# Optimization experiments

Measured on AMD Instinct MI355X. Metric: run time of the kernel, lower is better.

Reference implementation:

```python
import jax, jax.numpy as jnp
import numpy as np
from jax import lax

IMG = 256   # model img_size
O = 7       # adaptive pool output size (out_size)
R = 32      # number of ROIs
B = 8       # batch
CF = 32     # UNet output channels
FOUT = 512  # fc out_features


def _conv(x, w, b):
    y = lax.conv_general_dilated(x, w, (1, 1), 'SAME',
                                 dimension_numbers=('NCHW', 'OIHW', 'NCHW'))
    return y + b[None, :, None, None]


def _pool(x):
    return lax.reduce_window(x, -jnp.inf, lax.max, (1, 1, 2, 2), (1, 1, 2, 2), 'VALID')


def _up(x):
    return jnp.repeat(jnp.repeat(x, 2, axis=2), 2, axis=3)


def _unet(x, p):
    r = jax.nn.relu
    e1 = r(_conv(r(_conv(x, p['e1w1'], p['e1b1'])), p['e1w2'], p['e1b2']))          # [B,32,H,W]
    e2 = r(_conv(r(_conv(_pool(e1), p['e2w1'], p['e2b1'])), p['e2w2'], p['e2b2']))  # [B,64,H/2,W/2]
    bo = r(_conv(r(_conv(_pool(e2), p['bw1'], p['bb1'])), p['bw2'], p['bb2']))      # [B,128,H/4,W/4]
    u2 = r(_conv(_up(bo), p['u2w'], p['u2b']))                                      # [B,64,H/2,W/2]
    d2 = r(_conv(r(_conv(jnp.concatenate([u2, e2], 1), p['d2w1'], p['d2b1'])), p['d2w2'], p['d2b2']))
    u1 = r(_conv(_up(d2), p['u1w'], p['u1b']))                                      # [B,32,H,W]
    d1 = r(_conv(r(_conv(jnp.concatenate([u1, e1], 1), p['d1w1'], p['d1b1'])), p['d1w2'], p['d1b2']))
    return _conv(d1, p['fw'], p['fb'])                                              # [B,CF,H,W]


def _adaptive_pool(ii, boxes):
    # Exact F.adaptive_avg_pool2d bins via an integral image.
    # ii: [B,C,H+1,W+1] (zero-padded 2D cumsum); boxes: [R,4] int (x1,y1,x2,y2).
    i = jnp.arange(O)
    h = boxes[:, 3] - boxes[:, 1]
    w = boxes[:, 2] - boxes[:, 0]
    sy = boxes[:, 1:2] + (i[None, :] * h[:, None]) // O            # floor(i*h/O)
    ey = boxes[:, 1:2] + ((i[None, :] + 1) * h[:, None] + O - 1) // O  # ceil((i+1)*h/O)
    sx = boxes[:, 0:1] + (i[None, :] * w[:, None]) // O
    ex = boxes[:, 0:1] + ((i[None, :] + 1) * w[:, None] + O - 1) // O
    yA, yB = sy[:, :, None], ey[:, :, None]   # [R,O,1]
    xA, xB = sx[:, None, :], ex[:, None, :]   # [R,1,O]
    s = ii[:, :, yB, xB] - ii[:, :, yA, xB] - ii[:, :, yB, xA] + ii[:, :, yA, xA]  # [B,C,R,O,O]
    area = ((ey - sy)[:, :, None] * (ex - sx)[:, None, :]).astype(ii.dtype)        # [R,O,O]
    return s / area[None, None]


def _forward(x, rois, p):
    H, W = x.shape[2], x.shape[3]
    xs, ys = IMG // H, IMG // W  # matches torch: x_scale, y_scale = img_size//m, img_size//n
    boxes = rois // jnp.array([xs, ys, xs, ys], dtype=rois.dtype)
    f = _unet(x, p)                                   # [B,CF,H,W]
    ii = jnp.pad(jnp.cumsum(jnp.cumsum(f, axis=2), axis=3),
                 ((0, 0), (0, 0), (1, 0), (1, 0)))    # integral image [B,CF,H+1,W+1]
    rp = _adaptive_pool(ii, boxes)                    # [B,CF,R,O,O]
    roi_feat = jnp.transpose(rp, (0, 2, 1, 3, 4)).reshape(x.shape[0], boxes.shape[0] * f.shape[1], O, O)
    gbox = jnp.array([[0, 0, W, H]], dtype=boxes.dtype)
    gpool = _adaptive_pool(ii, gbox)[:, :, 0]         # [B,CF,O,O]
    out = jnp.concatenate([gpool, roi_feat], axis=1)  # [B,(R+1)*CF,O,O]
    out = out.reshape(out.shape[0], out.shape[1], O * O)
    return jnp.einsum('bnk,fk->bnf', out, p['fcw']) + p['fcb']


_PNAMES = ['e1w1','e1b1','e1w2','e1b2','e2w1','e2b1','e2w2','e2b2','bw1','bb1','bw2','bb2',
           'u2w','u2b','d2w1','d2b1','d2w2','d2b2','u1w','u1b','d1w1','d1b1','d1w2','d1b2',
           'fw','fb','fcw','fcb']


def setup_inputs() -> dict:
    key = jax.random.key(0)
    ks = jax.random.split(key, 32)

    def w(k, shape):
        fan = int(np.prod(shape[1:]))
        return jax.random.normal(k, shape, jnp.float32) * np.sqrt(2.0 / fan)

    d = {}
    d['x'] = jax.random.normal(ks[0], (B, 3, IMG, IMG), jnp.float32)
    xy1 = jax.random.randint(ks[1], (R, 2), 0, 192)
    wh = jax.random.randint(ks[2], (R, 2), 16, 64)
    d['rois'] = jnp.concatenate([xy1, xy1 + wh], axis=1).astype(jnp.int32)  # (x1,y1,x2,y2)

    shapes = {'e1w1': (32, 3, 3, 3), 'e1w2': (32, 32, 3, 3),
              'e2w1': (64, 32, 3, 3), 'e2w2': (64, 64, 3, 3),
              'bw1': (128, 64, 3, 3), 'bw2': (128, 128, 3, 3),
              'u2w': (64, 128, 3, 3),
              'd2w1': (64, 128, 3, 3), 'd2w2': (64, 64, 3, 3),
              'u1w': (32, 64, 3, 3),
              'd1w1': (32, 64, 3, 3), 'd1w2': (32, 32, 3, 3),
              'fw': (CF, 32, 1, 1),
              'fcw': (FOUT, O * O)}
    i = 3
    for n, s in shapes.items():
        d[n] = w(ks[i], s); i += 1
        bn = n.replace('w', 'b', 1) if 'w' in n else n
        d[bn] = jnp.zeros((s[0],), jnp.float32)
    d['fcb'] = jnp.zeros((FOUT,), jnp.float32)
    return d


def reference(x, rois, e1w1, e1b1, e1w2, e1b2, e2w1, e2b1, e2w2, e2b2,
              bw1, bb1, bw2, bb2, u2w, u2b, d2w1, d2b1, d2w2, d2b2,
              u1w, u1b, d1w1, d1b1, d1w2, d1b2, fw, fb, fcw, fcb):
    p = dict(e1w1=e1w1, e1b1=e1b1, e1w2=e1w2, e1b2=e1b2, e2w1=e2w1, e2b1=e2b1,
             e2w2=e2w2, e2b2=e2b2, bw1=bw1, bb1=bb1, bw2=bw2, bb2=bb2,
             u2w=u2w, u2b=u2b, d2w1=d2w1, d2b1=d2b1, d2w2=d2w2, d2b2=d2b2,
             u1w=u1w, u1b=u1b, d1w1=d1w1, d1b1=d1b1, d1w2=d1w2, d1b2=d1b2,
             fw=fw, fb=fb, fcw=fcw, fcb=fcb)
    return _forward(x, rois, p)
```

## Files before the change

kernel.cpp:

```cpp
#include <hip/hip_runtime.h>

typedef _Float16 half8 __attribute__((ext_vector_type(8)));
typedef float f32x4 __attribute__((ext_vector_type(4)));
typedef float f32x16 __attribute__((ext_vector_type(16)));

__device__ __forceinline__ unsigned short f2h(float f) {
    _Float16 h = (_Float16)f;
    return __builtin_bit_cast(unsigned short, h);
}
__device__ __forceinline__ float h2f(unsigned short u) {
    return (float)__builtin_bit_cast(_Float16, u);
}

__device__ __forceinline__ void lds_load16(const uint4* g, uint4* l) {
    __builtin_amdgcn_global_load_lds(
        (const __attribute__((address_space(1))) unsigned int*)g,
        (__attribute__((address_space(3))) unsigned int*)l, 16, 0, 0);
}

struct PrepArgs {
    const float* src[13];
    unsigned dstOff[13];
    int Cout[13], Cin[13];
    unsigned off[14];
};

__global__ void prep_all_k(PrepArgs a, char* __restrict__ WT)
{
    unsigned t = blockIdx.x * 256 + threadIdx.x;
    if (t >= a.off[13]) return;
    int l = 0;
    while (t >= a.off[l + 1]) ++l;
    unsigned e = t - a.off[l];
    if (l < 11) {
        int j = e & 7; unsigned r = e >> 3;
        const int Cout = a.Cout[l], Cin = a.Cin[l];
        int co = r % Cout; r /= Cout;
        int oct = r & 3; r >>= 2;
        int pos = r % 9; int ck = r / 9;
        int ci = ck * 32 + oct * 8 + j;
        ((unsigned short*)(WT + a.dstOff[l]))[e] =
            f2h(a.src[l][((size_t)co * Cin + ci) * 9 + pos]);
    } else if (l == 11) {
        int k = e >> 9, ff = e & 511;
        ((float*)(WT + a.dstOff[l]))[e] = a.src[l][ff * 49 + k];
    } else {
        int j = e & 7, co = (e >> 3) & 31, koct = e >> 8;
        ((unsigned short*)(WT + a.dstOff[l]))[e] =
            f2h(a.src[l][co * 32 + koct * 8 + j]);
    }
}

template<int BM, int TW, int TH, int LW, int UP, int POOL>
__global__ __launch_bounds__(256, 2) void convm4_k(
    const uint4* __restrict__ in1, int C1g,
    const uint4* __restrict__ in2, int C2g,
    const uint4* __restrict__ wt,
    const float* __restrict__ bias,
    unsigned short* __restrict__ out,
    int Cout, int relu, const uint4* __restrict__ zp,
    unsigned short* __restrict__ pout)
{
    constexpr int NM = BM / 16;
    constexpr int NN = (TW * TH) / 64;
    constexpr int CG = TW / 16;
    constexpr int RQ = NN / CG;
    static_assert(RQ == 2, "row-reuse layout needs 2 rows/wave");
    constexpr int Wf = 1 << LW, Hf = Wf;
    constexpr int WC = TW + 2, HR = TH + 2;
    constexpr int IN_GR = 4 * HR * WC;
    constexpr int LTW = (TW == 64) ? 6 : 5;
    constexpr int sH = UP ? (Hf >> 1) : Hf;
    constexpr int sW = UP ? (Wf >> 1) : Wf;
    __shared__ uint4 smem[IN_GR + 36 * BM];

    const int tid = threadIdx.x;
    const int lane = tid & 63, wv = tid >> 6;
    const int ng = Cout / BM;
    const int b = blockIdx.z / ng, cg = blockIdx.z % ng;
    const int x0 = blockIdx.x * TW, y0 = blockIdx.y * TH;
    const int NCK = (C1g + C2g) / 4;

    f32x4 acc[NM][NN];
#pragma unroll
    for (int m = 0; m < NM; ++m)
#pragma unroll
        for (int n = 0; n < NN; ++n) acc[m][n] = (f32x4){0.f, 0.f, 0.f, 0.f};

    const int l15 = lane & 15, l4 = lane >> 4;
    const int laneB = l4 * HR * WC + l15;
    const int laneA = l4 * BM + l15;

    for (int ck = 0; ck < NCK; ++ck) {
        if (ck) __syncthreads();
        {
            const uint4* src; int cg0, srcCg;
            if (ck * 4 < C1g) { src = in1; cg0 = ck * 4; srcCg = C1g; }
            else              { src = in2; cg0 = ck * 4 - C1g; srcCg = C2g; }
            for (int i = tid; i < IN_GR; i += 256) {
                int oct = i / (HR * WC);
                int rem = i - oct * (HR * WC);
                int row = rem / WC;
                int col = rem - row * WC;
                int gy = y0 + row - 1, gx = x0 + col - 1;
                int sy = UP ? (gy >> 1) : gy, sx = UP ? (gx >> 1) : gx;
                const uint4* ga = ((unsigned)gy < (unsigned)Hf && (unsigned)gx < (unsigned)Wf)
                    ? src + ((((size_t)b * sH + sy) * sW + sx) * srcCg + cg0 + oct)
                    : zp + (i & 63);
                lds_load16(ga, &smem[i]);
            }
        }
        {
            const uint4* wck = wt + (size_t)ck * 36 * Cout + (size_t)cg * BM;
            for (int i = tid; i < 36 * BM; i += 256) {
                int seg = i / BM, col = i - seg * BM;
                lds_load16(wck + seg * Cout + col, &smem[IN_GR + i]);
            }
        }
        __syncthreads();
        const half8* sB = (const half8*)smem;
        const half8* sA = (const half8*)(smem + IN_GR);
#pragma unroll
        for (int dc = 0; dc < 3; ++dc) {
            half8 br[RQ + 2][CG];
#pragma unroll
            for (int r = 0; r < RQ + 2; ++r)
#pragma unroll
                for (int c2 = 0; c2 < CG; ++c2)
                    br[r][c2] = sB[(wv * RQ + r) * WC + c2 * 16 + dc + laneB];
#pragma unroll
            for (int dr = 0; dr < 3; ++dr) {
                half8 af[NM];
#pragma unroll
                for (int m = 0; m < NM; ++m)
                    af[m] = sA[(dr * 3 + dc) * 4 * BM + m * 16 + laneA];
#pragma unroll
                for (int m = 0; m < NM; ++m)
#pragma unroll
                    for (int rq = 0; rq < RQ; ++rq)
#pragma unroll
                        for (int c2 = 0; c2 < CG; ++c2)
                            acc[m][rq * CG + c2] = __builtin_amdgcn_mfma_f32_16x16x32_f16(
                                af[m], br[rq + dr][c2], acc[m][rq * CG + c2], 0, 0, 0);
            }
        }
    }

#pragma unroll
    for (int m = 0; m < NM; ++m) {
        const int co0 = cg * BM + m * 16 + l4 * 4;
        const float4 bs = *(const float4*)(bias + co0);
#pragma unroll
        for (int c2 = 0; c2 < CG; ++c2) {
            float pv0, pv1, pv2, pv3;
#pragma unroll
            for (int rq = 0; rq < RQ; ++rq) {
                const int n = rq * CG + c2;
                const int pix = wv * (NN * 16) + n * 16 + l15;
                const int y = y0 + (pix >> LTW), x = x0 + (pix & (TW - 1));
                float v0 = acc[m][n][0] + bs.x;
                float v1 = acc[m][n][1] + bs.y;
                float v2 = acc[m][n][2] + bs.z;
                float v3 = acc[m][n][3] + bs.w;
                if (relu) {
                    v0 = fmaxf(v0, 0.f); v1 = fmaxf(v1, 0.f);
                    v2 = fmaxf(v2, 0.f); v3 = fmaxf(v3, 0.f);
                }
                uint2 pk;
                pk.x = (unsigned)f2h(v0) | ((unsigned)f2h(v1) << 16);
                pk.y = (unsigned)f2h(v2) | ((unsigned)f2h(v3) << 16);
                *(uint2*)(out + (((size_t)b * Hf + y) * Wf + x) * Cout + co0) = pk;
                if (POOL) {
                    if (rq == 0) { pv0 = v0; pv1 = v1; pv2 = v2; pv3 = v3; }
                    else {
                        pv0 = fmaxf(pv0, v0); pv1 = fmaxf(pv1, v1);
                        pv2 = fmaxf(pv2, v2); pv3 = fmaxf(pv3, v3);
                    }
                }
            }
            if (POOL) {
                float q0 = fmaxf(pv0, __shfl_xor(pv0, 1));
                float q1 = fmaxf(pv1, __shfl_xor(pv1, 1));
                float q2 = fmaxf(pv2, __shfl_xor(pv2, 1));
                float q3 = fmaxf(pv3, __shfl_xor(pv3, 1));
                if ((l15 & 1) == 0) {
                    const int xp = (x0 >> 1) + ((c2 * 16 + l15) >> 1);
                    const int yp = (y0 >> 1) + wv;
                    uint2 pk;
                    pk.x = (unsigned)f2h(q0) | ((unsigned)f2h(q1) << 16);
                    pk.y = (unsigned)f2h(q2) | ((unsigned)f2h(q3) << 16);
                    *(uint2*)(pout + (((size_t)b * (Hf >> 1) + yp) * (Wf >> 1) + xp) * Cout + co0) = pk;
                }
            }
        }
    }
}

__global__ __launch_bounds__(256) void conv0_k(
    const float* __restrict__ in, const float* __restrict__ w,
    const float* __restrict__ bias, unsigned short* __restrict__ out)
{
    __shared__ float s_in[3][18][18];
    const int tx = threadIdx.x, ty = threadIdx.y;
    const int tid = ty * 16 + tx;
    const int b = blockIdx.z >> 2;
    const int coBase = (blockIdx.z & 3) * 8;
    const int bx = blockIdx.x * 16, by = blockIdx.y * 16;

    for (int i = tid; i < 3 * 18 * 18; i += 256) {
        int cc = i / 324, r = i % 324;
        int ly = r / 18, lx = r % 18;
        int gy = by + ly - 1, gx = bx + lx - 1;
        float v = 0.f;
        if ((unsigned)gy < 256u && (unsigned)gx < 256u)
            v = in[(((size_t)(b * 3 + cc)) << 16) + (gy << 8) + gx];
        ((float*)s_in)[i] = v;
    }
    __syncthreads();
    float acc[8];
#pragma unroll
    for (int k = 0; k < 8; ++k) acc[k] = 0.f;
    for (int cc = 0; cc < 3; ++cc) {
        float v[9];
#pragma unroll
        for (int dh = 0; dh < 3; ++dh)
#pragma unroll
            for (int dw = 0; dw < 3; ++dw)
                v[dh * 3 + dw] = s_in[cc][ty + dh][tx + dw];
        const float* wp = w + ((size_t)coBase * 3 + cc) * 9;
#pragma unroll
        for (int k = 0; k < 8; ++k) {
            const float* wk = wp + (size_t)k * 27;
            float a = acc[k];
#pragma unroll
            for (int j = 0; j < 9; ++j) a = fmaf(v[j], wk[j], a);
            acc[k] = a;
        }
    }
    const int h = by + ty, ww = bx + tx;
    unsigned short* op = out + (((size_t)(b * 256 + h)) * 256 + ww) * 32 + coBase;
#pragma unroll
    for (int k = 0; k < 8; ++k)
        op[k] = f2h(fmaxf(acc[k] + bias[coBase + k], 0.f));
}

__global__ __launch_bounds__(256) void conv1x1f_k(
    const uint4* __restrict__ in, const uint4* __restrict__ w16,
    const float* __restrict__ bias, unsigned short* __restrict__ f)
{
    __shared__ uint4 sIn[1024];
    __shared__ uint4 sW[128];
    __shared__ float sb[32];
    const int tid = threadIdx.x;
    const int lane = tid & 63, wv = tid >> 6;
    const int l31 = lane & 31, l5 = lane >> 5;
    const int y = blockIdx.x, b = blockIdx.y;

    const uint4* ip = in + (((size_t)b * 256 + y) * 256) * 4;
#pragma unroll
    for (int it = 0; it < 4; ++it)
        lds_load16(ip + tid + it * 256, &sIn[tid + it * 256]);
    if (tid < 128) lds_load16(w16 + tid, &sW[tid]);
    if (tid < 32) sb[tid] = bias[tid];
    __syncthreads();

    const half8* hW = (const half8*)sW;
    const half8* hIn = (const half8*)sIn;
    half8 af0 = hW[l5 * 32 + l31];
    half8 af1 = hW[(2 + l5) * 32 + l31];
    unsigned short* fp_ = f + ((size_t)b * 32) * 65536 + (size_t)y * 256;
#pragma unroll
    for (int g = 0; g < 2; ++g) {
        const int p0 = wv * 64 + g * 32;
        half8 bf0 = hIn[(p0 + l31) * 4 + l5];
        half8 bf1 = hIn[(p0 + l31) * 4 + 2 + l5];
        f32x16 acc;
#pragma unroll
        for (int q = 0; q < 16; ++q) acc[q] = 0.f;
        acc = __builtin_amdgcn_mfma_f32_32x32x16_f16(af0, bf0, acc, 0, 0, 0);
        acc = __builtin_amdgcn_mfma_f32_32x32x16_f16(af1, bf1, acc, 0, 0, 0);
#pragma unroll
        for (int r = 0; r < 16; ++r) {
            const int co = (r & 3) + 8 * (r >> 2) + 4 * l5;
            fp_[(size_t)co * 65536 + p0 + l31] = f2h(acc[r] + sb[co]);
        }
    }
}

__global__ __launch_bounds__(256) void gcol_k(
    const unsigned short* __restrict__ f, float* __restrict__ colsumG)
{
    const int ki = blockIdx.x;
    const int c  = blockIdx.y;
    const int b  = blockIdx.z;
    const int x  = threadIdx.x;
    const int sy = (ki * 256) / 7, ey = ((ki + 1) * 256 + 6) / 7;
    const unsigned short* pl = f + (size_t)(b * 32 + c) * 65536;
    float s = 0.f;
    for (int y = sy; y < ey; ++y)
        s += h2f(pl[(size_t)y * 256 + x]);
    colsumG[((size_t)(b * 32 + c) * 7 + ki) * 256 + x] = s;
}

__global__ __launch_bounds__(64) void gpool2_k(
    const float* __restrict__ colsumG, float* __restrict__ pooled)
{
    const int c = blockIdx.x, b = blockIdx.y;
    const int lane = threadIdx.x;
    if (lane >= 49) return;
    const int ki = lane / 7, kj = lane % 7;
    const int sy = (ki * 256) / 7, ey = ((ki + 1) * 256 + 6) / 7;
    const int sx = (kj * 256) / 7, ex = ((kj + 1) * 256 + 6) / 7;
    const float* cs = colsumG + ((size_t)(b * 32 + c) * 7 + ki) * 256;
    float s = 0.f;
    for (int x = sx; x < ex; ++x) s += cs[x];
    pooled[((size_t)b * 1056 + c) * 49 + lane] = s / (float)((ey - sy) * (ex - sx));
}

__global__ __launch_bounds__(64) void roi_k(
    const unsigned short* __restrict__ f, const int* __restrict__ rois,
    float* __restrict__ pooled)
{
    __shared__ float colsum[7][64];
    const int n = 32 + blockIdx.x, b = blockIdx.y;
    const int lane = threadIdx.x;
    const int r = (n - 32) >> 5;
    const int c = (n - 32) & 31;
    const int x1 = rois[r * 4 + 0], y1 = rois[r * 4 + 1];
    const int x2 = rois[r * 4 + 2], y2 = rois[r * 4 + 3];
    const int h = y2 - y1, w = x2 - x1;
    const unsigned short* pl = f + (size_t)(b * 32 + c) * 65536;
    if (lane < w) {
        const int x = x1 + lane;
#pragma unroll
        for (int ki = 0; ki < 7; ++ki) {
            const int sy = y1 + (ki * h) / 7, ey = y1 + ((ki + 1) * h + 6) / 7;
            float s = 0.f;
            for (int y = sy; y < ey; ++y)
                s += h2f(pl[(size_t)y * 256 + x]);
            colsum[ki][lane] = s;
        }
    }
    __syncthreads();
    if (lane >= 49) return;
    const int ki = lane / 7, kj = lane % 7;
    const int sy = y1 + (ki * h) / 7, ey = y1 + ((ki + 1) * h + 6) / 7;
    const int sxo = (kj * w) / 7, exo = ((kj + 1) * w + 6) / 7;
    float s = 0.f;
    for (int j = sxo; j < exo; ++j) s += colsum[ki][j];
    pooled[((size_t)b * 1056 + n) * 49 + lane] = s / (float)((ey - sy) * (exo - sxo));
}

__global__ __launch_bounds__(512) void fc_k(
    const float* __restrict__ pooled, const float* __restrict__ fcwT,
    const float* __restrict__ fcb, float* __restrict__ out)
{
    const int nt = blockIdx.x, b = blockIdx.y;
    const int f = threadIdx.x;
    float wr[49];
#pragma unroll
    for (int k = 0; k < 49; ++k) wr[k] = fcwT[k * 512 + f];
    const float base = fcb[f];
    const float* pr = pooled + ((size_t)b * 1056 + nt * 16) * 49;
    float* op = out + (((size_t)b * 1056 + nt * 16)) * 512 + f;
#pragma unroll
    for (int j = 0; j < 16; ++j) {
        float a = base;
#pragma unroll
        for (int k = 0; k < 49; ++k)
            a = fmaf(pr[j * 49 + k], wr[k], a);
        op[(size_t)j * 512] = a;
    }
}

extern "C" void kernel_launch(void* const* d_in, const int* in_sizes, int n_in,
                              void* d_out, int out_size, void* d_ws, size_t ws_size,
                              hipStream_t stream)
{
    const float* x    = (const float*)d_in[0];
    const int*   rois = (const int*)d_in[1];
    const float* e1w1 = (const float*)d_in[2];
    const float* e1b1 = (const float*)d_in[3];
    const float* e1w2 = (const float*)d_in[4];
    const float* e1b2 = (const float*)d_in[5];
    const float* e2w1 = (const float*)d_in[6];
    const float* e2b1 = (const float*)d_in[7];
    const float* e2w2 = (const float*)d_in[8];
    const float* e2b2 = (const float*)d_in[9];
    const float* bw1  = (const float*)d_in[10];
    const float* bb1  = (const float*)d_in[11];
    const float* bw2  = (const float*)d_in[12];
    const float* bb2  = (const float*)d_in[13];
    const float* u2w  = (const float*)d_in[14];
    const float* u2b  = (const float*)d_in[15];
    const float* d2w1 = (const float*)d_in[16];
    const float* d2b1 = (const float*)d_in[17];
    const float* d2w2 = (const float*)d_in[18];
    const float* d2b2 = (const float*)d_in[19];
    const float* u1w  = (const float*)d_in[20];
    const float* u1b  = (const float*)d_in[21];
    const float* d1w1 = (const float*)d_in[22];
    const float* d1b1 = (const float*)d_in[23];
    const float* d1w2 = (const float*)d_in[24];
    const float* d1b2 = (const float*)d_in[25];
    const float* fw   = (const float*)d_in[26];
    const float* fb   = (const float*)d_in[27];
    const float* fcw  = (const float*)d_in[28];
    const float* fcb  = (const float*)d_in[29];

    char* wsb = (char*)d_ws;
    char* WT = wsb;
    char* A  = wsb + 4194304;
    char* D  = A + 33554432;
    char* E  = D + 16777216;
    char* Bb = E + 16777216;
    char* C  = Bb + 33554432;
    char* F  = C + 8388608;
    float* fcwT   = (float*)(WT + 1179648);
    unsigned short* fw16 = (unsigned short*)(WT + 2097152);
    uint4* zp     = (uint4*)(WT + 4194304 - 8192);
    unsigned short* fpl = (unsigned short*)F;
    float* pooled = (float*)C;
    float* colsumG = (float*)(C + 2097152);
    hipMemsetAsync(zp, 0, 8192, stream);

    const float* wsrc[11] = {e1w2, e2w1, e2w2, bw1, bw2, u2w, d2w1, d2w2, u1w, d1w1, d1w2};
    const int wco[11] = {32, 64, 64, 128, 128, 64, 64, 64, 32, 32, 32};
    const int wci[11] = {32, 32, 64, 64, 128, 128, 128, 64, 64, 64, 32};
    size_t woff[11]; size_t o = 0;
    PrepArgs pa;
    unsigned eoff = 0;
    for (int i = 0; i < 11; ++i) {
        woff[i] = o; o += (size_t)wco[i] * wci[i] * 18;
        pa.src[i] = wsrc[i]; pa.dstOff[i] = (unsigned)woff[i];
        pa.Cout[i] = wco[i]; pa.Cin[i] = wci[i];
        pa.off[i] = eoff; eoff += (unsigned)(wco[i] * wci[i] * 9);
    }
    pa.src[11] = fcw; pa.dstOff[11] = 1179648; pa.Cout[11] = 0; pa.Cin[11] = 0;
    pa.off[11] = eoff; eoff += 49 * 512;
    pa.src[12] = fw; pa.dstOff[12] = 2097152; pa.Cout[12] = 0; pa.Cin[12] = 0;
    pa.off[12] = eoff; eoff += 4096;
    pa.off[13] = eoff;
    hipLaunchKernelGGL(prep_all_k, dim3((eoff + 255) / 256), dim3(256), 0, stream, pa, WT);
    auto WP = [&](int i) { return (const uint4*)(WT + woff[i]); };

    #define CV1(i1,C1,i2,C2,wi,bs,ot,Cout,up,rl,pl,po) \
        hipLaunchKernelGGL((convm4_k<32,32,8,8,up,pl>), dim3(8,32,8*((Cout)/32)), dim3(256), 0, stream, \
            (const uint4*)(i1), (C1)/8, (const uint4*)(i2), (C2)/8, WP(wi), bs, \
            (unsigned short*)(ot), Cout, rl, zp, (unsigned short*)(po))
    #define CV2(i1,C1,i2,C2,wi,bs,ot,Cout,up,rl,pl,po) \
        hipLaunchKernelGGL((convm4_k<64,32,8,7,up,pl>), dim3(4,16,8*((Cout)/64)), dim3(256), 0, stream, \
            (const uint4*)(i1), (C1)/8, (const uint4*)(i2), (C2)/8, WP(wi), bs, \
            (unsigned short*)(ot), Cout, rl, zp, (unsigned short*)(po))
    #define CV3(i1,C1,i2,C2,wi,bs,ot,Cout,up,rl) \
        hipLaunchKernelGGL((convm4_k<32,32,8,6,up,0>), dim3(2,8,8*((Cout)/32)), dim3(256), 0, stream, \
            (const uint4*)(i1), (C1)/8, (const uint4*)(i2), (C2)/8, WP(wi), bs, \
            (unsigned short*)(ot), Cout, rl, zp, (unsigned short*)nullptr)

    hipLaunchKernelGGL(conv0_k, dim3(16, 16, 32), dim3(16, 16), 0, stream,
                       x, e1w1, e1b1, (unsigned short*)A);
    CV1(A, 32, nullptr, 0, 0, e1b2, Bb, 32, 0, 1, 1, C);
    CV2(C, 32, nullptr, 0, 1, e2b1, A, 64, 0, 1, 0, nullptr);
    CV2(A, 64, nullptr, 0, 2, e2b2, D, 64, 0, 1, 1, C);
    CV3(C, 64, nullptr, 0, 3, bb1, E, 128, 0, 1);
    CV3(E, 128, nullptr, 0, 4, bb2, A, 128, 0, 1);
    CV2(A, 128, nullptr, 0, 5, u2b, E, 64, 1, 1, 0, nullptr);
    CV2(E, 64, D, 64, 6, d2b1, A, 64, 0, 1, 0, nullptr);
    CV2(A, 64, nullptr, 0, 7, d2b2, D, 64, 0, 1, 0, nullptr);
    CV1(D, 64, nullptr, 0, 8, u1b, A, 32, 1, 1, 0, nullptr);
    CV1(A, 32, Bb, 32, 9, d1b1, D, 32, 0, 1, 0, nullptr);
    CV1(D, 32, nullptr, 0, 10, d1b2, Bb, 32, 0, 1, 0, nullptr);
    hipLaunchKernelGGL(conv1x1f_k, dim3(256, 8), dim3(256), 0, stream,
                       (const uint4*)Bb, (const uint4*)fw16, fb, fpl);
    hipLaunchKernelGGL(gcol_k, dim3(7, 32, 8), dim3(256), 0, stream, fpl, colsumG);
    hipLaunchKernelGGL(roi_k, dim3(1024, 8), dim3(64), 0, stream, fpl, rois, pooled);
    hipLaunchKernelGGL(gpool2_k, dim3(32, 8), dim3(64), 0, stream, colsumG, pooled);
    hipLaunchKernelGGL(fc_k, dim3(66, 8), dim3(512), 0, stream,
                       pooled, fcwT, fcb, (float*)d_out);
    #undef CV1
    #undef CV2
    #undef CV3
}
```

Baseline: 354.0 us.

## Double-buffer LDS staging in conv kernel and shrink BM for mid layers

Adds a DB template flag to the MFMA conv kernel so the next channel chunk's input tile and weights are issued into a second LDS buffer while the current chunk is computed. The aim is to hide global-to-LDS load latency behind MFMA work. Layers with several channel chunks now use the double-buffered variant, and the 64-channel mid layers switch from BM=64 to BM=32 to keep LDS usage down and launch more blocks. The cost is double the LDS footprint, which may lower occupancy. The async loads into the other buffer also rely on the end-of-iteration barrier to be complete before that buffer is read.

```diff
diff --git a/kernel.cpp b/kernel.cpp
--- a/kernel.cpp
+++ b/kernel.cpp
@@ -51,8 +51,8 @@
     }
 }
 
-template<int BM, int TW, int TH, int LW, int UP, int POOL>
-__global__ __launch_bounds__(256, 2) void convm4_k(
+template<int BM, int TW, int TH, int LW, int UP, int POOL, int DB>
+__global__ __launch_bounds__(256, 2) void convm5_k(
     const uint4* __restrict__ in1, int C1g,
     const uint4* __restrict__ in2, int C2g,
     const uint4* __restrict__ wt,
@@ -69,10 +69,13 @@
     constexpr int Wf = 1 << LW, Hf = Wf;
     constexpr int WC = TW + 2, HR = TH + 2;
     constexpr int IN_GR = 4 * HR * WC;
+    constexpr int WT_GR = 36 * BM;
+    constexpr int CHUNK = IN_GR + WT_GR;
     constexpr int LTW = (TW == 64) ? 6 : 5;
     constexpr int sH = UP ? (Hf >> 1) : Hf;
     constexpr int sW = UP ? (Wf >> 1) : Wf;
-    __shared__ uint4 smem[IN_GR + 36 * BM];
+    constexpr int NBUF = DB ? 2 : 1;
+    __shared__ uint4 smem[NBUF][CHUNK];
 
     const int tid = threadIdx.x;
     const int lane = tid & 63, wv = tid >> 6;
@@ -91,35 +94,36 @@
     const int laneB = l4 * HR * WC + l15;
     const int laneA = l4 * BM + l15;
 
+    auto stage = [&](int ck, int par) {
+        const uint4* src; int cg0, srcCg;
+        if (ck * 4 < C1g) { src = in1; cg0 = ck * 4; srcCg = C1g; }
+        else              { src = in2; cg0 = ck * 4 - C1g; srcCg = C2g; }
+        for (int i = tid; i < IN_GR; i += 256) {
+            int oct = i / (HR * WC);
+            int rem = i - oct * (HR * WC);
+            int row = rem / WC;
+            int col = rem - row * WC;
+            int gy = y0 + row - 1, gx = x0 + col - 1;
+            int sy = UP ? (gy >> 1) : gy, sx = UP ? (gx >> 1) : gx;
+            const uint4* ga = ((unsigned)gy < (unsigned)Hf && (unsigned)gx < (unsigned)Wf)
+                ? src + ((((size_t)b * sH + sy) * sW + sx) * srcCg + cg0 + oct)
+                : zp + (i & 63);
+            lds_load16(ga, &smem[par][i]);
+        }
+        const uint4* wck = wt + (size_t)ck * 36 * Cout + (size_t)cg * BM;
+        for (int i = tid; i < WT_GR; i += 256) {
+            int seg = i / BM, col = i - seg * BM;
+            lds_load16(wck + seg * Cout + col, &smem[par][IN_GR + i]);
+        }
+    };
+
+    stage(0, 0);
+    __syncthreads();
     for (int ck = 0; ck < NCK; ++ck) {
-        if (ck) __syncthreads();
-        {
-            const uint4* src; int cg0, srcCg;
-            if (ck * 4 < C1g) { src = in1; cg0 = ck * 4; srcCg = C1g; }
-            else              { src = in2; cg0 = ck * 4 - C1g; srcCg = C2g; }
-            for (int i = tid; i < IN_GR; i += 256) {
-                int oct = i / (HR * WC);
-                int rem = i - oct * (HR * WC);
-                int row = rem / WC;
-                int col = rem - row * WC;
-                int gy = y0 + row - 1, gx = x0 + col - 1;
-                int sy = UP ? (gy >> 1) : gy, sx = UP ? (gx >> 1) : gx;
-                const uint4* ga = ((unsigned)gy < (unsigned)Hf && (unsigned)gx < (unsigned)Wf)
-                    ? src + ((((size_t)b * sH + sy) * sW + sx) * srcCg + cg0 + oct)
-                    : zp + (i & 63);
-                lds_load16(ga, &smem[i]);
-            }
-        }
-        {
-            const uint4* wck = wt + (size_t)ck * 36 * Cout + (size_t)cg * BM;
-            for (int i = tid; i < 36 * BM; i += 256) {
-                int seg = i / BM, col = i - seg * BM;
-                lds_load16(wck + seg * Cout + col, &smem[IN_GR + i]);
-            }
-        }
-        __syncthreads();
-        const half8* sB = (const half8*)smem;
-        const half8* sA = (const half8*)(smem + IN_GR);
+        const int par = DB ? (ck & 1) : 0;
+        if (DB && ck + 1 < NCK) stage(ck + 1, par ^ 1);
+        const half8* sB = (const half8*)smem[par];
+        const half8* sA = (const half8*)(smem[par] + IN_GR);
 #pragma unroll
         for (int dc = 0; dc < 3; ++dc) {
             half8 br[RQ + 2][CG];
@@ -143,6 +147,10 @@
                             acc[m][rq * CG + c2] = __builtin_amdgcn_mfma_f32_16x16x32_f16(
                                 af[m], br[rq + dr][c2], acc[m][rq * CG + c2], 0, 0, 0);
             }
+        }
+        if (ck + 1 < NCK) {
+            if (!DB) { __syncthreads(); stage(ck + 1, 0); }
+            __syncthreads();
         }
     }
 
@@ -444,32 +452,40 @@
     hipLaunchKernelGGL(prep_all_k, dim3((eoff + 255) / 256), dim3(256), 0, stream, pa, WT);
     auto WP = [&](int i) { return (const uint4*)(WT + woff[i]); };
 
-    #define CV1(i1,C1,i2,C2,wi,bs,ot,Cout,up,rl,pl,po) \
-        hipLaunchKernelGGL((convm4_k<32,32,8,8,up,pl>), dim3(8,32,8*((Cout)/32)), dim3(256), 0, stream, \
+    #define CV1S(i1,C1,i2,C2,wi,bs,ot,Cout,up,rl,pl,po) \
+        hipLaunchKernelGGL((convm5_k<32,32,8,8,up,pl,0>), dim3(8,32,8*((Cout)/32)), dim3(256), 0, stream, \
             (const uint4*)(i1), (C1)/8, (const uint4*)(i2), (C2)/8, WP(wi), bs, \
             (unsigned short*)(ot), Cout, rl, zp, (unsigned short*)(po))
-    #define CV2(i1,C1,i2,C2,wi,bs,ot,Cout,up,rl,pl,po) \
-        hipLaunchKernelGGL((convm4_k<64,32,8,7,up,pl>), dim3(4,16,8*((Cout)/64)), dim3(256), 0, stream, \
+    #define CV1D(i1,C1,i2,C2,wi,bs,ot,Cout,up,rl,pl,po) \
+        hipLaunchKernelGGL((convm5_k<32,32,8,8,up,pl,1>), dim3(8,32,8*((Cout)/32)), dim3(256), 0, stream, \
             (const uint4*)(i1), (C1)/8, (const uint4*)(i2), (C2)/8, WP(wi), bs, \
             (unsigned short*)(ot), Cout, rl, zp, (unsigned short*)(po))
-    #define CV3(i1,C1,i2,C2,wi,bs,ot,Cout,up,rl) \
-        hipLaunchKernelGGL((convm4_k<32,32,8,6,up,0>), dim3(2,8,8*((Cout)/32)), dim3(256), 0, stream, \
+    #define CV2S(i1,C1,i2,C2,wi,bs,ot,Cout,up,rl,pl,po) \
+        hipLaunchKernelGGL((convm5_k<64,32,8,7,up,pl,0>), dim3(4,16,8*((Cout)/64)), dim3(256), 0, stream, \
+            (const uint4*)(i1), (C1)/8, (const uint4*)(i2), (C2)/8, WP(wi), bs, \
+            (unsigned short*)(ot), Cout, rl, zp, (unsigned short*)(po))
+    #define CV2D(i1,C1,i2,C2,wi,bs,ot,Cout,up,rl,pl,po) \
+        hipLaunchKernelGGL((convm5_k<32,32,8,7,up,pl,1>), dim3(4,16,8*((Cout)/32)), dim3(256), 0, stream, \
+            (const uint4*)(i1), (C1)/8, (const uint4*)(i2), (C2)/8, WP(wi), bs, \
+            (unsigned short*)(ot), Cout, rl, zp, (unsigned short*)(po))
+    #define CV3D(i1,C1,i2,C2,wi,bs,ot,Cout,up,rl) \
+        hipLaunchKernelGGL((convm5_k<32,32,8,6,up,0,1>), dim3(2,8,8*((Cout)/32)), dim3(256), 0, stream, \
             (const uint4*)(i1), (C1)/8, (const uint4*)(i2), (C2)/8, WP(wi), bs, \
             (unsigned short*)(ot), Cout, rl, zp, (unsigned short*)nullptr)
 
     hipLaunchKernelGGL(conv0_k, dim3(16, 16, 32), dim3(16, 16), 0, stream,
                        x, e1w1, e1b1, (unsigned short*)A);
-    CV1(A, 32, nullptr, 0, 0, e1b2, Bb, 32, 0, 1, 1, C);
-    CV2(C, 32, nullptr, 0, 1, e2b1, A, 64, 0, 1, 0, nullptr);
-    CV2(A, 64, nullptr, 0, 2, e2b2, D, 64, 0, 1, 1, C);
-    CV3(C, 64, nullptr, 0, 3, bb1, E, 128, 0, 1);
-    CV3(E, 128, nullptr, 0, 4, bb2, A, 128, 0, 1);
-    CV2(A, 128, nullptr, 0, 5, u2b, E, 64, 1, 1, 0, nullptr);
-    CV2(E, 64, D, 64, 6, d2b1, A, 64, 0, 1, 0, nullptr);
-    CV2(A, 64, nullptr, 0, 7, d2b2, D, 64, 0, 1, 0, nullptr);
-    CV1(D, 64, nullptr, 0, 8, u1b, A, 32, 1, 1, 0, nullptr);
-    CV1(A, 32, Bb, 32, 9, d1b1, D, 32, 0, 1, 0, nullptr);
-    CV1(D, 32, nullptr, 0, 10, d1b2, Bb, 32, 0, 1, 0, nullptr);
+    CV1S(A, 32, nullptr, 0, 0, e1b2, Bb, 32, 0, 1, 1, C);
+    CV2S(C, 32, nullptr, 0, 1, e2b1, A, 64, 0, 1, 0, nullptr);
+    CV2D(A, 64, nullptr, 0, 2, e2b2, D, 64, 0, 1, 1, C);
+    CV3D(C, 64, nullptr, 0, 3, bb1, E, 128, 0, 1);
+    CV3D(E, 128, nullptr, 0, 4, bb2, A, 128, 0, 1);
+    CV2D(A, 128, nullptr, 0, 5, u2b, E, 64, 1, 1, 0, nullptr);
+    CV2D(E, 64, D, 64, 6, d2b1, A, 64, 0, 1, 0, nullptr);
+    CV2D(A, 64, nullptr, 0, 7, d2b2, D, 64, 0, 1, 0, nullptr);
+    CV1D(D, 64, nullptr, 0, 8, u1b, A, 32, 1, 1, 0, nullptr);
+    CV1D(A, 32, Bb, 32, 9, d1b1, D, 32, 0, 1, 0, nullptr);
+    CV1S(D, 32, nullptr, 0, 10, d1b2, Bb, 32, 0, 1, 0, nullptr);
     hipLaunchKernelGGL(conv1x1f_k, dim3(256, 8), dim3(256), 0, stream,
                        (const uint4*)Bb, (const uint4*)fw16, fb, fpl);
     hipLaunchKernelGGL(gcol_k, dim3(7, 32, 8), dim3(256), 0, stream, fpl, colsumG);
@@ -477,7 +493,9 @@
     hipLaunchKernelGGL(gpool2_k, dim3(32, 8), dim3(64), 0, stream, colsumG, pooled);
     hipLaunchKernelGGL(fc_k, dim3(66, 8), dim3(512), 0, stream,
                        pooled, fcwT, fcb, (float*)d_out);
-    #undef CV1
-    #undef CV2
-    #undef CV3
-}
+    #undef CV1S
+    #undef CV1D
+    #undef CV2S
+    #undef CV2D
+    #undef CV3D
+}
```

Measured after the change: 373.5 us. 5.5% more time.
